# Performance work log

Hardware: AMD Instinct MI355X
Metric: run time of the kernel (lower is better)

The kernel has to match this reference:

```python
import jax, jax.numpy as jnp
import numpy as np

B, S, E = 2, 2048, 1024
H, KV, D = 16, 4, 64
GC = 128          # ve_gate_channels
EPS = 1.1920929e-07  # torch F.rms_norm default eps for fp32
NEG = -1e30


def setup_inputs() -> dict:
    key = jax.random.key(0)
    ks = jax.random.split(key, 8)
    x = jax.random.normal(ks[0], (B, S, E), jnp.float32)
    ve = jax.random.normal(ks[1], (B, S, KV * D), jnp.float32)
    half = D // 2
    inv_freq = 1.0 / (10000.0 ** (np.arange(half, dtype=np.float64) / half))
    ang = np.arange(S, dtype=np.float64)[:, None] * inv_freq[None, :]
    cos = jnp.asarray(np.cos(ang), jnp.float32)[:, None, :]  # [S,1,D/2]
    sin = jnp.asarray(np.sin(ang), jnp.float32)[:, None, :]
    sc = E ** -0.5
    Wq = jax.random.normal(ks[2], (E, H * D), jnp.float32) * sc
    Wk = jax.random.normal(ks[3], (E, KV * D), jnp.float32) * sc
    Wv = jax.random.normal(ks[4], (E, KV * D), jnp.float32) * sc
    Wproj = jax.random.normal(ks[5], (E, E), jnp.float32) * sc
    Wgate = jax.random.normal(ks[6], (GC, KV), jnp.float32) * (GC ** -0.5)
    return {"x": x, "ve": ve, "cos": cos, "sin": sin, "Wq": Wq, "Wk": Wk,
            "Wv": Wv, "Wproj": Wproj, "Wgate": Wgate,
            "window_left": 1024, "window_right": 0}


def _rms(x):
    return x * jax.lax.rsqrt(jnp.mean(x * x, axis=-1, keepdims=True) + EPS)


def _rope(x, cos, sin):
    d = x.shape[-1] // 2
    x1, x2 = x[..., :d], x[..., d:]
    return jnp.concatenate([x1 * cos + x2 * sin, -x1 * sin + x2 * cos], axis=-1)


def reference(x, ve, cos, sin, Wq, Wk, Wv, Wproj, Wgate, window_left, window_right):
    b, s, e = x.shape
    q = (x @ Wq).reshape(b, s, H, D)
    k = (x @ Wk).reshape(b, s, KV, D)
    v = (x @ Wv).reshape(b, s, KV, D)
    # value-embedding gate: 2*sigmoid over first GC channels, per kv-head
    gate = 2.0 * jax.nn.sigmoid(x[..., :GC] @ Wgate)          # [B,S,KV]
    v = v + gate[..., None] * ve.reshape(b, s, KV, D)
    q = _rms(_rope(q, cos, sin))
    k = _rms(_rope(k, cos, sin))
    # GQA: repeat kv heads to match query heads
    g = H // KV
    kk = jnp.repeat(k, g, axis=2)                             # [B,S,H,D]
    vv = jnp.repeat(v, g, axis=2)
    scores = jnp.einsum('bihd,bjhd->bhij', q, kk) * (D ** -0.5)
    i = jnp.arange(s)[:, None]
    j = jnp.arange(s)[None, :]
    mask = (j <= i + window_right) & (j >= i - window_left) & (j <= i)
    scores = jnp.where(mask, scores, NEG)
    p = jax.nn.softmax(scores, axis=-1)
    y = jnp.einsum('bhij,bjhd->bihd', p, vv).reshape(b, s, H * D)
    return y @ Wproj
```

## Files before the change

kernel.cpp:

```cpp
#include <hip/hip_runtime.h>

typedef __bf16 bf16;
typedef __bf16 bf16x4 __attribute__((ext_vector_type(4)));
typedef __bf16 bf16x8 __attribute__((ext_vector_type(8)));
typedef float floatx4 __attribute__((ext_vector_type(4)));

#define EPS 1.1920929e-07f
#define QSCALE (0.125f * 1.44269504088896f)
#define SHIFT_C 11.5416f

__device__ __forceinline__ floatx4 mfma16(bf16x8 a, bf16x8 b, floatx4 c) {
  return __builtin_amdgcn_mfma_f32_16x16x32_bf16(a, b, c, 0, 0, 0);
}

__device__ __forceinline__ void gload16(const void* g, void* l) {
  __builtin_amdgcn_global_load_lds((const __attribute__((address_space(1))) unsigned int*)g,
                                   (__attribute__((address_space(3))) unsigned int*)l, 16, 0, 0);
}

__global__ void prep_kernel(const float* __restrict__ x, const float* __restrict__ wgate,
                            const float* __restrict__ Wq, const float* __restrict__ Wk,
                            const float* __restrict__ Wv, const float* __restrict__ Wproj,
                            bf16* __restrict__ xb, float* __restrict__ gate,
                            bf16* __restrict__ out_qkv, bf16* __restrict__ out_proj) {
  __shared__ float tile[32][33];
  const int tid = threadIdx.x;
  if (blockIdx.x < 4096) {
    int t = blockIdx.x;
    const float* xr = x + (size_t)t * 1024;
    float4 v = *(const float4*)(xr + tid * 4);
    bf16x4 o = {(bf16)v.x, (bf16)v.y, (bf16)v.z, (bf16)v.w};
    *(bf16x4*)(xb + (size_t)t * 1024 + tid * 4) = o;
    if (tid < 64) {
      int c = (tid & 31) * 4;
#pragma unroll
      for (int kv = 0; kv < 4; kv++) {
        float g = v.x * wgate[(c + 0) * 4 + kv] + v.y * wgate[(c + 1) * 4 + kv] +
                  v.z * wgate[(c + 2) * 4 + kv] + v.w * wgate[(c + 3) * 4 + kv];
        g += __shfl_xor(g, 1, 64);
        g += __shfl_xor(g, 2, 64);
        g += __shfl_xor(g, 4, 64);
        g += __shfl_xor(g, 8, 64);
        g += __shfl_xor(g, 16, 64);
        if (tid == 0) {
          int b = t >> 11, s = t & 2047;
          gate[((size_t)b * 4 + kv) * 2048 + s] = 2.f / (1.f + __expf(-g));
        }
      }
    }
  } else {
    int j = blockIdx.x - 4096;
    int ky = j / 80;
    int nx = j - ky * 80;
    int k0 = ky * 32;
    int tx = tid & 31, ty = tid >> 5;
    if (nx < 48) {
      int n0 = nx * 32;
#pragma unroll
      for (int i = 0; i < 4; i++) {
        int k = k0 + ty + i * 8, n = n0 + tx;
        float v;
        if (n < 1024)      v = Wq[(size_t)k * 1024 + n];
        else if (n < 1280) v = Wk[(size_t)k * 256 + (n - 1024)];
        else               v = Wv[(size_t)k * 256 + (n - 1280)];
        tile[ty + i * 8][tx] = v;
      }
      __syncthreads();
#pragma unroll
      for (int i = 0; i < 4; i++) {
        int n = n0 + ty + i * 8, k = k0 + tx;
        out_qkv[(size_t)n * 1024 + k] = (bf16)tile[tx][ty + i * 8];
      }
    } else {
      int n0 = (nx - 48) * 32;
#pragma unroll
      for (int i = 0; i < 4; i++)
        tile[ty + i * 8][tx] = Wproj[(size_t)(k0 + ty + i * 8) * 1024 + n0 + tx];
      __syncthreads();
#pragma unroll
      for (int i = 0; i < 4; i++)
        out_proj[(size_t)(n0 + ty + i * 8) * 1024 + k0 + tx] = (bf16)tile[tx][ty + i * 8];
    }
  }
}

__global__ __launch_bounds__(256) void qkv_gemm_kernel(const bf16* __restrict__ A,
                                                       const bf16* __restrict__ Bt,
                                                       const float* __restrict__ ve,
                                                       const float* __restrict__ cosb,
                                                       const float* __restrict__ sinb,
                                                       const float* __restrict__ gate,
                                                       bf16* __restrict__ Qb,
                                                       bf16* __restrict__ Kf,
                                                       bf16* __restrict__ Vf) {
  __shared__ __align__(16) char smem[24576];
  bf16* As = (bf16*)smem;
  bf16* Bs = (bf16*)(smem + 16384);
  bf16* Ep = (bf16*)smem;
  const int K = 1024;
  const int tid = threadIdx.x;
  const int tile = blockIdx.x;
  const int m0 = blockIdx.y * 128, n0 = tile * 64;
  const int w = tid >> 6, lane = tid & 63;
  const int q = lane >> 4, r0 = lane & 15;
  const int lrow = lane >> 2, lcol = (lane & 3) * 8;
  const int b = m0 >> 11, s0 = m0 & 2047;

  floatx4 acc[2][4];
#pragma unroll
  for (int i = 0; i < 2; i++)
#pragma unroll
    for (int j = 0; j < 4; j++) acc[i][j] = (floatx4){0.f, 0.f, 0.f, 0.f};

  for (int k0 = 0; k0 < K; k0 += 64) {
    __syncthreads();
#pragma unroll
    for (int i = 0; i < 4; i++) {
      int g = w * 4 + i, s = g >> 3, rb = g & 7;
      gload16(A + (size_t)(m0 + rb * 16 + lrow) * K + k0 + s * 32 + lcol, &As[s * 4096 + rb * 512]);
    }
#pragma unroll
    for (int i = 0; i < 2; i++) {
      int g = w * 2 + i, s = g >> 2, rb = g & 3;
      gload16(Bt + (size_t)(n0 + rb * 16 + lrow) * K + k0 + s * 32 + lcol, &Bs[s * 2048 + rb * 512]);
    }
    __syncthreads();
#pragma unroll
    for (int s = 0; s < 2; s++) {
      bf16x8 af[2], bfr[4];
#pragma unroll
      for (int mt = 0; mt < 2; mt++) af[mt] = *(const bf16x8*)&As[s * 4096 + (w * 32 + mt * 16 + r0) * 32 + q * 8];
#pragma unroll
      for (int nt = 0; nt < 4; nt++) bfr[nt] = *(const bf16x8*)&Bs[s * 2048 + (nt * 16 + r0) * 32 + q * 8];
#pragma unroll
      for (int mt = 0; mt < 2; mt++)
#pragma unroll
        for (int nt = 0; nt < 4; nt++)
          acc[mt][nt] = mfma16(af[mt], bfr[nt], acc[mt][nt]);
    }
  }
  __syncthreads();

  if (tile < 16) {
    const int h = tile;
#pragma unroll
    for (int mt = 0; mt < 2; mt++) {
      float rvv[4][4];
#pragma unroll
      for (int ntp = 0; ntp < 2; ntp++) {
        int d31 = ntp * 16 + r0;
#pragma unroll
        for (int r = 0; r < 4; r++) {
          int s = s0 + w * 32 + mt * 16 + q * 4 + r;
          float c = cosb[s * 32 + d31], sn = sinb[s * 32 + d31];
          float v1 = acc[mt][ntp][r], v2 = acc[mt][ntp + 2][r];
          rvv[ntp][r] = v1 * c + v2 * sn;
          rvv[ntp + 2][r] = v2 * c - v1 * sn;
        }
      }
#pragma unroll
      for (int r = 0; r < 4; r++) {
        float ss = 0.f;
#pragma unroll
        for (int nt = 0; nt < 4; nt++) ss += rvv[nt][r] * rvv[nt][r];
        ss += __shfl_xor(ss, 1, 64);
        ss += __shfl_xor(ss, 2, 64);
        ss += __shfl_xor(ss, 4, 64);
        ss += __shfl_xor(ss, 8, 64);
        float sc = rsqrtf(ss * (1.f / 64.f) + EPS) * QSCALE;
        int row = w * 32 + mt * 16 + q * 4 + r;
#pragma unroll
        for (int nt = 0; nt < 4; nt++)
          Ep[row * 72 + nt * 16 + r0] = (bf16)(rvv[nt][r] * sc);
      }
    }
    __syncthreads();
#pragma unroll
    for (int p = 0; p < 4; p++) {
      int g = p * 256 + tid;
      int row = g >> 3, chunk = g & 7;
      *(uint4*)&Qb[(((size_t)b * 16 + h) * 2048 + s0 + row) * 64 + chunk * 8] =
          *(const uint4*)&Ep[row * 72 + chunk * 8];
    }
  } else if (tile < 20) {
    const int kv = tile - 16;
#pragma unroll
    for (int mt = 0; mt < 2; mt++) {
      float rvv[4][4];
#pragma unroll
      for (int ntp = 0; ntp < 2; ntp++) {
        int d31 = ntp * 16 + r0;
#pragma unroll
        for (int r = 0; r < 4; r++) {
          int s = s0 + w * 32 + mt * 16 + q * 4 + r;
          float c = cosb[s * 32 + d31], sn = sinb[s * 32 + d31];
          float v1 = acc[mt][ntp][r], v2 = acc[mt][ntp + 2][r];
          rvv[ntp][r] = v1 * c + v2 * sn;
          rvv[ntp + 2][r] = v2 * c - v1 * sn;
        }
      }
#pragma unroll
      for (int r = 0; r < 4; r++) {
        float ss = 0.f;
#pragma unroll
        for (int nt = 0; nt < 4; nt++) ss += rvv[nt][r] * rvv[nt][r];
        ss += __shfl_xor(ss, 1, 64);
        ss += __shfl_xor(ss, 2, 64);
        ss += __shfl_xor(ss, 4, 64);
        ss += __shfl_xor(ss, 8, 64);
        float sc = rsqrtf(ss * (1.f / 64.f) + EPS);
        int row = w * 32 + mt * 16 + q * 4 + r;
#pragma unroll
        for (int nt = 0; nt < 4; nt++)
          Ep[row * 72 + nt * 16 + r0] = (bf16)(rvv[nt][r] * sc);
      }
    }
    __syncthreads();
    {
      int tk = (s0 >> 5) + w;
      size_t tb = ((size_t)(b * 4 + kv) * 64 + tk) * 2048;
#pragma unroll
      for (int u = 0; u < 4; u++) {
        int joff = (u >= 2) ? 16 : 0, doff = (u & 1) * 32;
        bf16x8 f = *(const bf16x8*)&Ep[(w * 32 + joff + r0) * 72 + doff + q * 8];
        *(bf16x8*)&Kf[tb + u * 512 + lane * 8] = f;
      }
    }
  } else {
    const int kv = tile - 20;
    const float* gbase = gate + ((size_t)b * 4 + kv) * 2048;
#pragma unroll
    for (int mt = 0; mt < 2; mt++) {
#pragma unroll
      for (int r = 0; r < 4; r++) {
        int row = w * 32 + mt * 16 + q * 4 + r;
        float gg = gbase[s0 + row];
#pragma unroll
        for (int nt = 0; nt < 4; nt++) {
          int d = nt * 16 + r0;
          float vv = acc[mt][nt][r] + gg * ve[(size_t)(m0 + row) * 256 + kv * 64 + d];
          Ep[row * 72 + d] = (bf16)vv;
        }
      }
    }
    __syncthreads();
    {
      int tk = (s0 >> 5) + w;
      size_t tb = ((size_t)(b * 4 + kv) * 64 + tk) * 2048;
#pragma unroll
      for (int nt = 0; nt < 4; nt++) {
        bf16 tmp[8];
#pragma unroll
        for (int e = 0; e < 8; e++) {
          int jl = w * 32 + (e >> 2) * 16 + 4 * q + (e & 3);
          tmp[e] = Ep[jl * 72 + nt * 16 + r0];
        }
        *(uint4*)&Vf[tb + nt * 512 + lane * 8] = *(uint4*)tmp;
      }
    }
  }
}

__global__ __launch_bounds__(256) void proj_gemm_kernel(const bf16* __restrict__ A,
                                                        const bf16* __restrict__ Bt,
                                                        float* __restrict__ Cout) {
  __shared__ __align__(16) bf16 As[2 * 128 * 32];
  __shared__ __align__(16) bf16 Bs[2 * 64 * 32];
  const int K = 1024, N = 1024;
  const int tid = threadIdx.x;
  const int m0 = blockIdx.y * 128, n0 = blockIdx.x * 64;
  const int w = tid >> 6, lane = tid & 63;
  const int q = lane >> 4, r0 = lane & 15;
  const int lrow = lane >> 2, lcol = (lane & 3) * 8;

  floatx4 acc[2][4];
#pragma unroll
  for (int i = 0; i < 2; i++)
#pragma unroll
    for (int j = 0; j < 4; j++) acc[i][j] = (floatx4){0.f, 0.f, 0.f, 0.f};

  for (int k0 = 0; k0 < K; k0 += 64) {
    __syncthreads();
#pragma unroll
    for (int i = 0; i < 4; i++) {
      int g = w * 4 + i, s = g >> 3, rb = g & 7;
      gload16(A + (size_t)(m0 + rb * 16 + lrow) * K + k0 + s * 32 + lcol, &As[s * 4096 + rb * 512]);
    }
#pragma unroll
    for (int i = 0; i < 2; i++) {
      int g = w * 2 + i, s = g >> 2, rb = g & 3;
      gload16(Bt + (size_t)(n0 + rb * 16 + lrow) * K + k0 + s * 32 + lcol, &Bs[s * 2048 + rb * 512]);
    }
    __syncthreads();
#pragma unroll
    for (int s = 0; s < 2; s++) {
      bf16x8 af[2], bfr[4];
#pragma unroll
      for (int mt = 0; mt < 2; mt++) af[mt] = *(const bf16x8*)&As[s * 4096 + (w * 32 + mt * 16 + r0) * 32 + q * 8];
#pragma unroll
      for (int nt = 0; nt < 4; nt++) bfr[nt] = *(const bf16x8*)&Bs[s * 2048 + (nt * 16 + r0) * 32 + q * 8];
#pragma unroll
      for (int mt = 0; mt < 2; mt++)
#pragma unroll
        for (int nt = 0; nt < 4; nt++)
          acc[mt][nt] = mfma16(af[mt], bfr[nt], acc[mt][nt]);
    }
  }
#pragma unroll
  for (int mt = 0; mt < 2; mt++)
#pragma unroll
    for (int nt = 0; nt < 4; nt++)
#pragma unroll
      for (int r = 0; r < 4; r++) {
        int row = m0 + w * 32 + mt * 16 + q * 4 + r;
        int col = n0 + nt * 16 + r0;
        Cout[(size_t)row * N + col] = acc[mt][nt][r];
      }
}

__global__ __launch_bounds__(256, 4) void attn_kernel(const bf16* __restrict__ Qb,
                                                      const bf16* __restrict__ Kf,
                                                      const bf16* __restrict__ Vf,
                                                      const int* __restrict__ wlp,
                                                      const int* __restrict__ wrp,
                                                      bf16* __restrict__ Yb) {
  const int wl = wlp[0];
  const int wrc = min(wrp[0], 0);
  const int blk = blockIdx.x;
  const int bkv = blk & 7;
  const int b = bkv >> 2, kvh = bkv & 3;
  const int cm = 127 - (blk >> 3);
  const int w = threadIdx.x >> 6, lane = threadIdx.x & 63;
  const int q = lane >> 4, r0 = lane & 15;
  const int h = kvh * 4 + w;
  const int q0 = cm << 4;

  const bf16* qbase = Qb + (((size_t)b * 16 + h) * 2048 + q0 + r0) * 64;
  bf16x8 aq0 = *(const bf16x8*)(qbase + q * 8);
  bf16x8 aq1 = *(const bf16x8*)(qbase + 32 + q * 8);

  floatx4 O[4];
#pragma unroll
  for (int nt = 0; nt < 4; nt++) O[nt] = (floatx4){0.f, 0.f, 0.f, 0.f};
  floatx4 L = (floatx4){0.f, 0.f, 0.f, 0.f};

  const bf16 onev = (bf16)1.0f;
  const bf16x8 ones = {onev, onev, onev, onev, onev, onev, onev, onev};

  const int jlo = max(0, q0 - wl) & ~31;
  const int jhi = q0 + 15 + wrc;
  const int count = ((jhi - jlo) >> 5) + 1;
  const int tile0 = jlo >> 5;

  const bf16* kfb = Kf + ((size_t)(b * 4 + kvh) * 64) * 2048 + lane * 8;
  const bf16* vfb = Vf + ((size_t)(b * 4 + kvh) * 64) * 2048 + lane * 8;

  bf16x8 kf[4], vf[4], nk[4], nv[4];
#pragma unroll
  for (int u = 0; u < 4; u++) {
    kf[u] = *(const bf16x8*)(kfb + (size_t)tile0 * 2048 + u * 512);
    vf[u] = *(const bf16x8*)(vfb + (size_t)tile0 * 2048 + u * 512);
  }

  for (int t = 0; t < count; t++) {
    const int j0 = jlo + (t << 5);
    const int tn = (t + 1 < count) ? tile0 + t + 1 : tile0 + t;
#pragma unroll
    for (int u = 0; u < 4; u++) {
      nk[u] = *(const bf16x8*)(kfb + (size_t)tn * 2048 + u * 512);
      nv[u] = *(const bf16x8*)(vfb + (size_t)tn * 2048 + u * 512);
    }

    floatx4 s0 = (floatx4){-SHIFT_C, -SHIFT_C, -SHIFT_C, -SHIFT_C};
    floatx4 s1 = s0;
    __builtin_amdgcn_s_setprio(1);
    s0 = mfma16(kf[0], aq0, s0);
    s0 = mfma16(kf[1], aq1, s0);
    s1 = mfma16(kf[2], aq0, s1);
    s1 = mfma16(kf[3], aq1, s1);
    __builtin_amdgcn_s_setprio(0);

    bf16x8 pa;
    if (j0 >= q0 + 15 - wl && j0 + 31 <= q0 + wrc) {
#pragma unroll
      for (int r = 0; r < 4; r++) {
        pa[r] = (bf16)exp2f(s0[r]);
        pa[4 + r] = (bf16)exp2f(s1[r]);
      }
    } else {
      const int i = q0 + r0;
#pragma unroll
      for (int r = 0; r < 4; r++) {
        int ja = j0 + 4 * q + r, jb = ja + 16;
        bool va = (ja <= i + wrc) && (ja >= i - wl);
        bool vb = (jb <= i + wrc) && (jb >= i - wl);
        pa[r] = va ? (bf16)exp2f(s0[r]) : (bf16)0.f;
        pa[4 + r] = vb ? (bf16)exp2f(s1[r]) : (bf16)0.f;
      }
    }

    __builtin_amdgcn_s_setprio(1);
    L = mfma16(pa, ones, L);
#pragma unroll
    for (int nt = 0; nt < 4; nt++) O[nt] = mfma16(pa, vf[nt], O[nt]);
    __builtin_amdgcn_s_setprio(0);

#pragma unroll
    for (int u = 0; u < 4; u++) { kf[u] = nk[u]; vf[u] = nv[u]; }
  }

  float inv[4];
#pragma unroll
  for (int r = 0; r < 4; r++) inv[r] = 1.f / L[r];
#pragma unroll
  for (int nt = 0; nt < 4; nt++)
#pragma unroll
    for (int r = 0; r < 4; r++) {
      int i = q0 + q * 4 + r;
      Yb[((size_t)b * 2048 + i) * 1024 + h * 64 + nt * 16 + r0] = (bf16)(O[nt][r] * inv[r]);
    }
}

extern "C" void kernel_launch(void* const* d_in, const int* in_sizes, int n_in,
                              void* d_out, int out_size, void* d_ws, size_t ws_size,
                              hipStream_t stream) {
  const float* x     = (const float*)d_in[0];
  const float* ve    = (const float*)d_in[1];
  const float* cosb  = (const float*)d_in[2];
  const float* sinb  = (const float*)d_in[3];
  const float* Wq    = (const float*)d_in[4];
  const float* Wk    = (const float*)d_in[5];
  const float* Wv    = (const float*)d_in[6];
  const float* Wproj = (const float*)d_in[7];
  const float* Wgate = (const float*)d_in[8];
  const int* wl      = (const int*)d_in[9];
  const int* wr      = (const int*)d_in[10];

  char* ws = (char*)d_ws;
  bf16* Xb      = (bf16*)(ws);
  bf16* Wqkv_t  = (bf16*)(ws + 8388608);
  bf16* Wproj_t = (bf16*)(ws + 11534336);
  bf16* Qb      = (bf16*)(ws + 13631488);
  bf16* Kf      = (bf16*)(ws + 22020096);
  bf16* Vf      = (bf16*)(ws + 24117248);
  bf16* Yb      = (bf16*)(ws + 26214400);
  float* gateb  = (float*)(ws + 34603008);

  prep_kernel<<<4096 + 2560, 256, 0, stream>>>(x, Wgate, Wq, Wk, Wv, Wproj, Xb, gateb, Wqkv_t, Wproj_t);
  qkv_gemm_kernel<<<dim3(24, 32), 256, 0, stream>>>(Xb, Wqkv_t, ve, cosb, sinb, gateb, Qb, Kf, Vf);
  attn_kernel<<<1024, 256, 0, stream>>>(Qb, Kf, Vf, wl, wr, Yb);
  proj_gemm_kernel<<<dim3(16, 32), 256, 0, stream>>>(Yb, Wproj_t, (float*)d_out);
}
```

Baseline: 167.3 us.

## Remap GEMM block IDs for XCD locality and shorten V prefetch in attention

Both GEMM kernels now use a 1D grid whose block index is remapped so that consecutive blocks on the same XCD (blockIdx mod 8) cover contiguous output tiles. This is meant to improve L2 reuse of A and B tiles across MI355X's chiplets. The attention loop now loads V for the current tile at the start of each iteration instead of double-buffering it, which cuts register pressure and may raise occupancy. The risk is that V load latency is exposed before the PV MFMAs.

```diff
diff --git a/kernel.cpp b/kernel.cpp
--- a/kernel.cpp
+++ b/kernel.cpp
@@ -99,8 +99,10 @@
   bf16* Ep = (bf16*)smem;
   const int K = 1024;
   const int tid = threadIdx.x;
-  const int tile = blockIdx.x;
-  const int m0 = blockIdx.y * 128, n0 = tile * 64;
+  const int orig = blockIdx.x;
+  const int lid = (orig & 7) * 96 + (orig >> 3);
+  const int tile = lid % 24;
+  const int m0 = (lid / 24) * 128, n0 = tile * 64;
   const int w = tid >> 6, lane = tid & 63;
   const int q = lane >> 4, r0 = lane & 15;
   const int lrow = lane >> 2, lcol = (lane & 3) * 8;
@@ -268,7 +270,9 @@
   __shared__ __align__(16) bf16 Bs[2 * 64 * 32];
   const int K = 1024, N = 1024;
   const int tid = threadIdx.x;
-  const int m0 = blockIdx.y * 128, n0 = blockIdx.x * 64;
+  const int orig = blockIdx.x;
+  const int lid = (orig & 7) * 64 + (orig >> 3);
+  const int m0 = (lid / 16) * 128, n0 = (lid % 16) * 64;
   const int w = tid >> 6, lane = tid & 63;
   const int q = lane >> 4, r0 = lane & 15;
   const int lrow = lane >> 2, lcol = (lane & 3) * 8;
@@ -355,21 +359,19 @@
   const bf16* kfb = Kf + ((size_t)(b * 4 + kvh) * 64) * 2048 + lane * 8;
   const bf16* vfb = Vf + ((size_t)(b * 4 + kvh) * 64) * 2048 + lane * 8;
 
-  bf16x8 kf[4], vf[4], nk[4], nv[4];
-#pragma unroll
-  for (int u = 0; u < 4; u++) {
+  bf16x8 kf[4], nk[4], vf[4];
+#pragma unroll
+  for (int u = 0; u < 4; u++)
     kf[u] = *(const bf16x8*)(kfb + (size_t)tile0 * 2048 + u * 512);
-    vf[u] = *(const bf16x8*)(vfb + (size_t)tile0 * 2048 + u * 512);
-  }
 
   for (int t = 0; t < count; t++) {
     const int j0 = jlo + (t << 5);
-    const int tn = (t + 1 < count) ? tile0 + t + 1 : tile0 + t;
-#pragma unroll
-    for (int u = 0; u < 4; u++) {
-      nk[u] = *(const bf16x8*)(kfb + (size_t)tn * 2048 + u * 512);
-      nv[u] = *(const bf16x8*)(vfb + (size_t)tn * 2048 + u * 512);
-    }
+    const int tcur = tile0 + t;
+    const int tn = (t + 1 < count) ? tcur + 1 : tcur;
+#pragma unroll
+    for (int u = 0; u < 4; u++) nk[u] = *(const bf16x8*)(kfb + (size_t)tn * 2048 + u * 512);
+#pragma unroll
+    for (int u = 0; u < 4; u++) vf[u] = *(const bf16x8*)(vfb + (size_t)tcur * 2048 + u * 512);
 
     floatx4 s0 = (floatx4){-SHIFT_C, -SHIFT_C, -SHIFT_C, -SHIFT_C};
     floatx4 s1 = s0;
@@ -406,7 +408,7 @@
     __builtin_amdgcn_s_setprio(0);
 
 #pragma unroll
-    for (int u = 0; u < 4; u++) { kf[u] = nk[u]; vf[u] = nv[u]; }
+    for (int u = 0; u < 4; u++) kf[u] = nk[u];
   }
 
   float inv[4];
@@ -447,7 +449,7 @@
   float* gateb  = (float*)(ws + 34603008);
 
   prep_kernel<<<4096 + 2560, 256, 0, stream>>>(x, Wgate, Wq, Wk, Wv, Wproj, Xb, gateb, Wqkv_t, Wproj_t);
-  qkv_gemm_kernel<<<dim3(24, 32), 256, 0, stream>>>(Xb, Wqkv_t, ve, cosb, sinb, gateb, Qb, Kf, Vf);
+  qkv_gemm_kernel<<<768, 256, 0, stream>>>(Xb, Wqkv_t, ve, cosb, sinb, gateb, Qb, Kf, Vf);
   attn_kernel<<<1024, 256, 0, stream>>>(Qb, Kf, Vf, wl, wr, Yb);
-  proj_gemm_kernel<<<dim3(16, 32), 256, 0, stream>>>(Yb, Wproj_t, (float*)d_out);
-}
+  proj_gemm_kernel<<<512, 256, 0, stream>>>(Yb, Wproj_t, (float*)d_out);
+}
```

Result: no change. 166.1 us (-0.7%).
